# Optimization experiments

Hardware: AMD Instinct MI355X
Metric: run time of the kernel (lower is better)

The kernel has to match this reference:

```python
import jax, jax.numpy as jnp
import numpy as np

EMBED_DIM = 768
NUM_HEADS = 12
HEAD_DIM = EMBED_DIM // NUM_HEADS
B, S = 2, 2048


def setup_inputs() -> dict:
    key = jax.random.key(0)
    k1, k2, k3, k4, k5 = jax.random.split(key, 5)
    scale = 1.0 / np.sqrt(EMBED_DIM)
    return {
        "x": jax.random.normal(k1, (B, S, EMBED_DIM), dtype=jnp.float32),
        "w_qkv": jax.random.normal(k2, (EMBED_DIM, 3 * EMBED_DIM), dtype=jnp.float32) * scale,
        "b_qkv": jax.random.normal(k3, (3 * EMBED_DIM,), dtype=jnp.float32) * 0.01,
        "w_proj": jax.random.normal(k4, (EMBED_DIM, EMBED_DIM), dtype=jnp.float32) * scale,
        "b_proj": jax.random.normal(k5, (EMBED_DIM,), dtype=jnp.float32) * 0.01,
    }


def reference(x, w_qkv, b_qkv, w_proj, b_proj):
    b, s, e = x.shape
    h, d = NUM_HEADS, HEAD_DIM
    # fused QKV projection: [b, s, 3, h, d]
    qkv = (x @ w_qkv + b_qkv).reshape(b, s, 3, h, d)
    q = qkv[:, :, 0].transpose(0, 2, 1, 3)  # [b, h, s, d]
    k = qkv[:, :, 1].transpose(0, 2, 1, 3)
    v = qkv[:, :, 2].transpose(0, 2, 1, 3)
    scores = jnp.einsum("bhqd,bhkd->bhqk", q, k) * (d ** -0.5)
    attn = jax.nn.softmax(scores, axis=-1)  # dropout is identity in eval mode
    out = jnp.einsum("bhqk,bhkd->bhqd", attn, v)
    out = out.transpose(0, 2, 1, 3).reshape(b, s, e)
    return out @ w_proj + b_proj
```

## Files before the change

### kernel.cpp

```cpp
#include <hip/hip_runtime.h>
#include <hip/hip_bf16.h>


typedef __bf16 bf16x8 __attribute__((ext_vector_type(8)));
typedef float f32x4 __attribute__((ext_vector_type(4)));
typedef unsigned short ushortx8 __attribute__((ext_vector_type(8)));
typedef unsigned short ushortx4 __attribute__((ext_vector_type(4)));

#define EMB 768
#define SEQ 2048
#define NHEAD 12
#define HDIM 64
#define MROWS 4096
#define NQKV 2304
#define QSCALE 0.18033688011112042f

static __device__ __forceinline__ unsigned short b16(float f) {
  __hip_bfloat16 h = __float2bfloat16(f);
  return __builtin_bit_cast(unsigned short, h);
}

static __device__ __forceinline__ void gld16(const void* g, void* l) {
  __builtin_amdgcn_global_load_lds((const __attribute__((address_space(1))) void*)g,
                                   (__attribute__((address_space(3))) void*)l, 16, 0, 0);
}

__global__ __launch_bounds__(256) void k_prep(
    const float* __restrict__ x, const float* __restrict__ wqkv, const float* __restrict__ wproj,
    unsigned short* __restrict__ xb, unsigned short* __restrict__ wqkvT,
    unsigned short* __restrict__ wprojT) {
  __shared__ float t[64][65];
  const int bid = blockIdx.x;
  if (bid < 3072) {
    int i = (bid * 256 + threadIdx.x) * 4;
    f32x4 v = *(const f32x4*)(x + i);
    ushortx4 o;
    o[0] = b16(v[0]); o[1] = b16(v[1]); o[2] = b16(v[2]); o[3] = b16(v[3]);
    *(ushortx4*)(xb + i) = o;
    return;
  }
  const float* in; unsigned short* out; int N, bx, by;
  if (bid < 3072 + 432) { in = wqkv;  out = wqkvT;  N = NQKV; int r = bid - 3072; bx = r % 36; by = r / 36; }
  else                  { in = wproj; out = wprojT; N = EMB;  int r = bid - 3504; bx = r % 12; by = r / 12; }
  const int n0 = bx * 64, k0 = by * 64;
  const int xx = threadIdx.x & 63, y0 = threadIdx.x >> 6;
  #pragma unroll
  for (int i = 0; i < 16; ++i) { int r = y0 * 16 + i; t[r][xx] = in[(size_t)(k0 + r) * N + n0 + xx]; }
  __syncthreads();
  #pragma unroll
  for (int i = 0; i < 16; ++i) { int r = y0 * 16 + i; out[(size_t)(n0 + r) * EMB + k0 + xx] = b16(t[xx][r]); }
}

static __device__ __forceinline__ void gemm_tile_128(
    const unsigned short* __restrict__ A, const unsigned short* __restrict__ B,
    int K, int bm, int bn, char* lA, char* lB, f32x4 acc[4][4]) {
  const int tid = threadIdx.x, lane = tid & 63, w = tid >> 6;
  const int l15 = lane & 15, lg = lane >> 4;
  const int wm = w >> 1, wn = w & 1;
  #pragma unroll
  for (int m = 0; m < 4; ++m)
    #pragma unroll
    for (int n = 0; n < 4; ++n)
      acc[m][n] = (f32x4){0.f, 0.f, 0.f, 0.f};

  const size_t aoff1 = (size_t)(bm * 128 + (tid >> 2)) * K + (tid & 3) * 8;
  const size_t aoff2 = aoff1 + (size_t)64 * K;
  const size_t boff1 = (size_t)(bn * 128 + (tid >> 2)) * K + (tid & 3) * 8;
  const size_t boff2 = boff1 + (size_t)64 * K;
  const char* aBase = lA + (wm * 64 + l15) * 64 + lg * 16;
  const char* bBase = lB + (wn * 64 + l15) * 64 + lg * 16;
  const int T = K >> 5;

  #define GSTAGE(tt, buf) do {                                   \
    char* ad_ = lA + (buf) * 8192 + w * 1024;                    \
    char* bd_ = lB + (buf) * 8192 + w * 1024;                    \
    const int k0_ = (tt) << 5;                                   \
    gld16(A + aoff1 + k0_, ad_);                                 \
    gld16(A + aoff2 + k0_, ad_ + 4096);                          \
    gld16(B + boff1 + k0_, bd_);                                 \
    gld16(B + boff2 + k0_, bd_ + 4096);                          \
  } while (0)

  GSTAGE(0, 0);
  GSTAGE(1, 1);
  asm volatile("s_waitcnt vmcnt(4)" ::: "memory");
  __builtin_amdgcn_s_barrier();

  int cur = 0, pre = 2;
  for (int t = 0; t < T; ++t) {
    if (t + 2 < T) GSTAGE(t + 2, pre);
    const char* ab = aBase + cur * 8192;
    const char* bb = bBase + cur * 8192;
    bf16x8 af[4], bfr[4];
    #pragma unroll
    for (int m = 0; m < 4; ++m) af[m] = *(const bf16x8*)(ab + m * 1024);
    #pragma unroll
    for (int n = 0; n < 4; ++n) bfr[n] = *(const bf16x8*)(bb + n * 1024);
    __builtin_amdgcn_s_setprio(1);
    #pragma unroll
    for (int m = 0; m < 4; ++m)
      #pragma unroll
      for (int n = 0; n < 4; ++n)
        acc[m][n] = __builtin_amdgcn_mfma_f32_16x16x32_bf16(af[m], bfr[n], acc[m][n], 0, 0, 0);
    __builtin_amdgcn_s_setprio(0);
    if (t + 1 < T) {
      if (t + 2 < T) asm volatile("s_waitcnt vmcnt(4)" ::: "memory");
      else           asm volatile("s_waitcnt vmcnt(0)" ::: "memory");
      __builtin_amdgcn_s_barrier();
    }
    cur = (cur == 2) ? 0 : cur + 1;
    pre = (pre == 2) ? 0 : pre + 1;
  }
  #undef GSTAGE
}

static __device__ __forceinline__ int kvperm(int s) {
  return (s & ~0x1C) | ((s & 0x0C) << 1) | ((s & 0x10) >> 2);
}

__global__ __launch_bounds__(256) void k_gemm_qkv(
    const unsigned short* __restrict__ Xb, const unsigned short* __restrict__ Wt,
    const float* __restrict__ bias,
    unsigned short* __restrict__ Qb, unsigned short* __restrict__ Kb,
    unsigned short* __restrict__ VTb) {
  __shared__ __align__(16) char Alds[3 * 8192];
  __shared__ __align__(16) char Blds[3 * 8192];
  f32x4 acc[4][4];
  const int bm = blockIdx.x, bn = blockIdx.y;
  gemm_tile_128(Xb, Wt, EMB, bm, bn, Alds, Blds, acc);
  const int tid = threadIdx.x, lane = tid & 63, w = tid >> 6;
  const int l15 = lane & 15, lg = lane >> 4, wm = w >> 1, wn = w & 1;
  const int treg = bn / 6;
  if (treg < 2) {
    #pragma unroll
    for (int m = 0; m < 4; ++m)
      #pragma unroll
      for (int n = 0; n < 4; ++n)
        #pragma unroll
        for (int r = 0; r < 4; ++r) {
          int gr = bm * 128 + wm * 64 + m * 16 + lg * 4 + r;
          int gc = bn * 128 + wn * 64 + n * 16 + l15;
          float v = acc[m][n][r] + bias[gc];
          int rem = gc - treg * 768;
          int h = rem >> 6, d = rem & 63;
          int b = gr >> 11, s = gr & 2047;
          size_t off = ((size_t)(b * 12 + h) * 2048 + s) * 64 + d;
          if (treg == 0) Qb[off] = b16(v * QSCALE);
          else           Kb[off] = b16(v);
        }
  } else {
    #pragma unroll
    for (int m = 0; m < 4; ++m)
      #pragma unroll
      for (int n = 0; n < 4; ++n) {
        int gr0 = bm * 128 + wm * 64 + m * 16 + lg * 4;
        int gc = bn * 128 + wn * 64 + n * 16 + l15;
        int rem = gc - 1536;
        int h = rem >> 6, d = rem & 63;
        int b = gr0 >> 11, s0 = gr0 & 2047;
        int sp0 = kvperm(s0);
        ushortx4 o;
        #pragma unroll
        for (int r = 0; r < 4; ++r) o[r] = b16(acc[m][n][r] + bias[gc]);
        *(ushortx4*)(VTb + ((size_t)(b * 12 + h) * 64 + d) * 2048 + sp0) = o;
      }
  }
}

__global__ __launch_bounds__(256) void k_gemm_proj(
    const unsigned short* __restrict__ Ab, const unsigned short* __restrict__ Wt,
    const float* __restrict__ bias, float* __restrict__ out) {
  __shared__ __align__(16) char Alds[3 * 8192];
  __shared__ __align__(16) char Blds[3 * 8192];
  f32x4 acc[4][4];
  const int bm = blockIdx.x, bn = blockIdx.y;
  gemm_tile_128(Ab, Wt, EMB, bm, bn, Alds, Blds, acc);
  const int tid = threadIdx.x, lane = tid & 63, w = tid >> 6;
  const int l15 = lane & 15, lg = lane >> 4, wm = w >> 1, wn = w & 1;
  #pragma unroll
  for (int m = 0; m < 4; ++m)
    #pragma unroll
    for (int n = 0; n < 4; ++n)
      #pragma unroll
      for (int r = 0; r < 4; ++r) {
        int gr = bm * 128 + wm * 64 + m * 16 + lg * 4 + r;
        int gc = bn * 128 + wn * 64 + n * 16 + l15;
        out[(size_t)gr * EMB + gc] = acc[m][n][r] + bias[gc];
      }
}

__global__ __launch_bounds__(256) void k_attn(
    const unsigned short* __restrict__ Qg, const unsigned short* __restrict__ Kg,
    const unsigned short* __restrict__ VTg, unsigned short* __restrict__ AO) {
  __shared__ __align__(16) char KL[3 * 8192];
  __shared__ __align__(16) char VTL[3 * 8192];
  const int bid = blockIdx.x;
  const int bh = bid >> 5, qt = bid & 31;
  const int b = bh / 12, h = bh % 12;
  const size_t base = (size_t)bh * (SEQ * HDIM);
  const int tid = threadIdx.x, lane = tid & 63, w = tid >> 6;
  const int l15 = lane & 15, lg = lane >> 4;
  const int swz = (l15 & 7) << 4;

  bf16x8 qf[2];
  {
    const size_t qoff = base + (size_t)(qt * 64 + w * 16 + l15) * 64 + lg * 8;
    qf[0] = *(const bf16x8*)(Qg + qoff);
    qf[1] = *(const bf16x8*)(Qg + qoff + 32);
  }

  const int srow0 = tid >> 3;
  const int scg0 = (tid & 7) ^ (srow0 & 7);
  const int scg1 = (tid & 7) ^ ((srow0 + 32) & 7);

  #define ASTAGE(tt, buf) do {                                                         \
    const int kv_ = (tt) * 64;                                                         \
    char* kd_ = KL + (buf) * 8192 + w * 1024;                                          \
    char* vd_ = VTL + (buf) * 8192 + w * 1024;                                         \
    gld16(Kg + base + (size_t)(kv_ + srow0) * 64 + scg0 * 8,           kd_);           \
    gld16(Kg + base + (size_t)(kv_ + srow0 + 32) * 64 + scg1 * 8,      kd_ + 4096);    \
    gld16(VTg + base + (size_t)srow0 * 2048 + kv_ + scg0 * 8,          vd_);           \
    gld16(VTg + base + (size_t)(srow0 + 32) * 2048 + kv_ + scg1 * 8,   vd_ + 4096);    \
  } while (0)

  f32x4 Oacc[4];
  #pragma unroll
  for (int nd = 0; nd < 4; ++nd) Oacc[nd] = (f32x4){0.f, 0.f, 0.f, 0.f};
  float l_ = 0.f;

  ASTAGE(0, 0);
  ASTAGE(1, 1);
  asm volatile("s_waitcnt vmcnt(4)" ::: "memory");
  __builtin_amdgcn_s_barrier();

  int cur = 0, pre = 2;
  for (int t = 0; t < 32; ++t) {
    if (t + 2 < 32) ASTAGE(t + 2, pre);
    const char* kb = KL + cur * 8192;
    const char* vb = VTL + cur * 8192;

    f32x4 sv[4];
    __builtin_amdgcn_s_setprio(1);
    #pragma unroll
    for (int n = 0; n < 4; ++n) {
      const char* rb = kb + (n * 16 + l15) * 128;
      bf16x8 kf0 = *(const bf16x8*)(rb + ((lg * 16) ^ swz));
      bf16x8 kf1 = *(const bf16x8*)(rb + ((64 + lg * 16) ^ swz));
      f32x4 z = (f32x4){0.f, 0.f, 0.f, 0.f};
      z = __builtin_amdgcn_mfma_f32_16x16x32_bf16(kf0, qf[0], z, 0, 0, 0);
      sv[n] = __builtin_amdgcn_mfma_f32_16x16x32_bf16(kf1, qf[1], z, 0, 0, 0);
    }

    #pragma unroll
    for (int c = 0; c < 2; ++c) {
      ushortx8 up;
      #pragma unroll
      for (int j = 0; j < 4; ++j) {
        float pa = __builtin_amdgcn_exp2f(sv[2 * c][j]);
        float pb = __builtin_amdgcn_exp2f(sv[2 * c + 1][j]);
        l_ += pa + pb;
        up[j] = b16(pa);
        up[4 + j] = b16(pb);
      }
      bf16x8 pfB = __builtin_bit_cast(bf16x8, up);
      #pragma unroll
      for (int nd = 0; nd < 4; ++nd) {
        const char* vr = vb + (nd * 16 + l15) * 128;
        bf16x8 vf = *(const bf16x8*)(vr + ((c * 64 + lg * 16) ^ swz));
        Oacc[nd] = __builtin_amdgcn_mfma_f32_16x16x32_bf16(vf, pfB, Oacc[nd], 0, 0, 0);
      }
    }
    __builtin_amdgcn_s_setprio(0);

    if (t < 31) {
      if (t < 30) asm volatile("s_waitcnt vmcnt(4)" ::: "memory");
      else        asm volatile("s_waitcnt vmcnt(0)" ::: "memory");
      __builtin_amdgcn_s_barrier();
    }
    cur = (cur == 2) ? 0 : cur + 1;
    pre = (pre == 2) ? 0 : pre + 1;
  }
  #undef ASTAGE

  l_ += __shfl_xor(l_, 16);
  l_ += __shfl_xor(l_, 32);
  const float rl = 1.0f / l_;
  const int q = qt * 64 + w * 16 + l15;
  #pragma unroll
  for (int nd = 0; nd < 4; ++nd) {
    ushortx4 o;
    #pragma unroll
    for (int r = 0; r < 4; ++r) o[r] = b16(Oacc[nd][r] * rl);
    *(ushortx4*)(AO + ((size_t)(b * 2048 + q)) * EMB + h * 64 + nd * 16 + lg * 4) = o;
  }
}

extern "C" void kernel_launch(void* const* d_in, const int* in_sizes, int n_in,
                              void* d_out, int out_size, void* d_ws, size_t ws_size,
                              hipStream_t stream) {
  const float* x     = (const float*)d_in[0];
  const float* wqkv  = (const float*)d_in[1];
  const float* bqkv  = (const float*)d_in[2];
  const float* wproj = (const float*)d_in[3];
  const float* bproj = (const float*)d_in[4];
  float* out = (float*)d_out;
  char* ws = (char*)d_ws;

  unsigned short* xb     = (unsigned short*)(ws + 0);
  unsigned short* wqkvT  = (unsigned short*)(ws + 6291456);
  unsigned short* wprojT = (unsigned short*)(ws + 9830400);
  unsigned short* Qb     = (unsigned short*)(ws + 11010048);
  unsigned short* Kb     = (unsigned short*)(ws + 17301504);
  unsigned short* VTb    = (unsigned short*)(ws + 23592960);
  unsigned short* AOb    = (unsigned short*)(ws + 29884416);

  k_prep<<<3648, 256, 0, stream>>>(x, wqkv, wproj, xb, wqkvT, wprojT);
  k_gemm_qkv<<<dim3(MROWS / 128, NQKV / 128), 256, 0, stream>>>(xb, wqkvT, bqkv, Qb, Kb, VTb);
  k_attn<<<24 * (SEQ / 64), 256, 0, stream>>>(Qb, Kb, VTb, AOb);
  k_gemm_proj<<<dim3(MROWS / 128, EMB / 128), 256, 0, stream>>>(AOb, wprojT, bproj, out);
}
```

Baseline: 106.6 us.

## Software-pipeline attention PV with next QK, remap blocks per XCD, unroll GEMM

The attention loop is restructured so the PV MFMAs for the previous tile overlap with the QK and exp work for the current tile. The row sum is now computed by an MFMA against a ones vector instead of VALU adds and shuffles. All three kernels remap block IDs so related tiles land on the same XCD (id&7), aiming at better L2 reuse. The GEMM K loop is fully unrolled with a compile-time K and setprio is dropped there. The costs are higher register pressure from holding the V fragments, and the row sum now accumulates bf16-rounded probabilities.

```diff
diff --git a/kernel.cpp b/kernel.cpp
--- a/kernel.cpp
+++ b/kernel.cpp
@@ -53,7 +53,7 @@
 
 static __device__ __forceinline__ void gemm_tile_128(
     const unsigned short* __restrict__ A, const unsigned short* __restrict__ B,
-    int K, int bm, int bn, char* lA, char* lB, f32x4 acc[4][4]) {
+    int bm, int bn, char* lA, char* lB, f32x4 acc[4][4]) {
   const int tid = threadIdx.x, lane = tid & 63, w = tid >> 6;
   const int l15 = lane & 15, lg = lane >> 4;
   const int wm = w >> 1, wn = w & 1;
@@ -63,13 +63,12 @@
     for (int n = 0; n < 4; ++n)
       acc[m][n] = (f32x4){0.f, 0.f, 0.f, 0.f};
 
-  const size_t aoff1 = (size_t)(bm * 128 + (tid >> 2)) * K + (tid & 3) * 8;
-  const size_t aoff2 = aoff1 + (size_t)64 * K;
-  const size_t boff1 = (size_t)(bn * 128 + (tid >> 2)) * K + (tid & 3) * 8;
-  const size_t boff2 = boff1 + (size_t)64 * K;
+  const size_t aoff1 = (size_t)(bm * 128 + (tid >> 2)) * EMB + (tid & 3) * 8;
+  const size_t aoff2 = aoff1 + (size_t)64 * EMB;
+  const size_t boff1 = (size_t)(bn * 128 + (tid >> 2)) * EMB + (tid & 3) * 8;
+  const size_t boff2 = boff1 + (size_t)64 * EMB;
   const char* aBase = lA + (wm * 64 + l15) * 64 + lg * 16;
   const char* bBase = lB + (wn * 64 + l15) * 64 + lg * 16;
-  const int T = K >> 5;
 
   #define GSTAGE(tt, buf) do {                                   \
     char* ad_ = lA + (buf) * 8192 + w * 1024;                    \
@@ -86,9 +85,10 @@
   asm volatile("s_waitcnt vmcnt(4)" ::: "memory");
   __builtin_amdgcn_s_barrier();
 
-  int cur = 0, pre = 2;
-  for (int t = 0; t < T; ++t) {
-    if (t + 2 < T) GSTAGE(t + 2, pre);
+  #pragma unroll
+  for (int t = 0; t < 24; ++t) {
+    const int cur = t % 3;
+    if (t + 2 < 24) GSTAGE(t + 2, (t + 2) % 3);
     const char* ab = aBase + cur * 8192;
     const char* bb = bBase + cur * 8192;
     bf16x8 af[4], bfr[4];
@@ -96,20 +96,16 @@
     for (int m = 0; m < 4; ++m) af[m] = *(const bf16x8*)(ab + m * 1024);
     #pragma unroll
     for (int n = 0; n < 4; ++n) bfr[n] = *(const bf16x8*)(bb + n * 1024);
-    __builtin_amdgcn_s_setprio(1);
     #pragma unroll
     for (int m = 0; m < 4; ++m)
       #pragma unroll
       for (int n = 0; n < 4; ++n)
         acc[m][n] = __builtin_amdgcn_mfma_f32_16x16x32_bf16(af[m], bfr[n], acc[m][n], 0, 0, 0);
-    __builtin_amdgcn_s_setprio(0);
-    if (t + 1 < T) {
-      if (t + 2 < T) asm volatile("s_waitcnt vmcnt(4)" ::: "memory");
-      else           asm volatile("s_waitcnt vmcnt(0)" ::: "memory");
+    if (t + 1 < 24) {
+      if (t + 2 < 24) asm volatile("s_waitcnt vmcnt(4)" ::: "memory");
+      else            asm volatile("s_waitcnt vmcnt(0)" ::: "memory");
       __builtin_amdgcn_s_barrier();
     }
-    cur = (cur == 2) ? 0 : cur + 1;
-    pre = (pre == 2) ? 0 : pre + 1;
   }
   #undef GSTAGE
 }
@@ -126,8 +122,11 @@
   __shared__ __align__(16) char Alds[3 * 8192];
   __shared__ __align__(16) char Blds[3 * 8192];
   f32x4 acc[4][4];
-  const int bm = blockIdx.x, bn = blockIdx.y;
-  gemm_tile_128(Xb, Wt, EMB, bm, bn, Alds, Blds, acc);
+  const int id = blockIdx.x;
+  const int k = id >> 3;
+  const int bn = k % 18;
+  const int bm = (id & 7) * 4 + k / 18;
+  gemm_tile_128(Xb, Wt, bm, bn, Alds, Blds, acc);
   const int tid = threadIdx.x, lane = tid & 63, w = tid >> 6;
   const int l15 = lane & 15, lg = lane >> 4, wm = w >> 1, wn = w & 1;
   const int treg = bn / 6;
@@ -173,8 +172,11 @@
   __shared__ __align__(16) char Alds[3 * 8192];
   __shared__ __align__(16) char Blds[3 * 8192];
   f32x4 acc[4][4];
-  const int bm = blockIdx.x, bn = blockIdx.y;
-  gemm_tile_128(Ab, Wt, EMB, bm, bn, Alds, Blds, acc);
+  const int id = blockIdx.x;
+  const int k = id >> 3;
+  const int bn = k % 6;
+  const int bm = (id & 7) * 4 + k / 6;
+  gemm_tile_128(Ab, Wt, bm, bn, Alds, Blds, acc);
   const int tid = threadIdx.x, lane = tid & 63, w = tid >> 6;
   const int l15 = lane & 15, lg = lane >> 4, wm = w >> 1, wn = w & 1;
   #pragma unroll
@@ -195,7 +197,9 @@
   __shared__ __align__(16) char KL[3 * 8192];
   __shared__ __align__(16) char VTL[3 * 8192];
   const int bid = blockIdx.x;
-  const int bh = bid >> 5, qt = bid & 31;
+  const int slot = bid >> 3;
+  const int bh = (bid & 7) * 3 + slot / 32;
+  const int qt = slot & 31;
   const int b = bh / 12, h = bh % 12;
   const size_t base = (size_t)bh * (SEQ * HDIM);
   const int tid = threadIdx.x, lane = tid & 63, w = tid >> 6;
@@ -223,68 +227,98 @@
     gld16(VTg + base + (size_t)(srow0 + 32) * 2048 + kv_ + scg1 * 8,   vd_ + 4096);    \
   } while (0)
 
+  ushortx8 os;
+  #pragma unroll
+  for (int j = 0; j < 8; ++j) os[j] = 0x3F80;
+  const bf16x8 onesf = __builtin_bit_cast(bf16x8, os);
+
   f32x4 Oacc[4];
   #pragma unroll
   for (int nd = 0; nd < 4; ++nd) Oacc[nd] = (f32x4){0.f, 0.f, 0.f, 0.f};
-  float l_ = 0.f;
+  f32x4 Lacc = (f32x4){0.f, 0.f, 0.f, 0.f};
+  bf16x8 pf0, pf1;
+  bf16x8 vf[8];
+
+  #define QK_EXP(kb_) do {                                                             \
+    f32x4 sv[4];                                                                       \
+    _Pragma("unroll")                                                                  \
+    for (int n = 0; n < 4; ++n) {                                                      \
+      const char* rb = (kb_) + (n * 16 + l15) * 128;                                   \
+      bf16x8 kf0 = *(const bf16x8*)(rb + ((lg * 16) ^ swz));                           \
+      bf16x8 kf1 = *(const bf16x8*)(rb + ((64 + lg * 16) ^ swz));                      \
+      f32x4 z = (f32x4){0.f, 0.f, 0.f, 0.f};                                           \
+      z = __builtin_amdgcn_mfma_f32_16x16x32_bf16(kf0, qf[0], z, 0, 0, 0);             \
+      sv[n] = __builtin_amdgcn_mfma_f32_16x16x32_bf16(kf1, qf[1], z, 0, 0, 0);         \
+    }                                                                                  \
+    ushortx8 u0, u1;                                                                   \
+    _Pragma("unroll")                                                                  \
+    for (int j = 0; j < 4; ++j) {                                                      \
+      u0[j]     = b16(__builtin_amdgcn_exp2f(sv[0][j]));                               \
+      u0[4 + j] = b16(__builtin_amdgcn_exp2f(sv[1][j]));                               \
+      u1[j]     = b16(__builtin_amdgcn_exp2f(sv[2][j]));                               \
+      u1[4 + j] = b16(__builtin_amdgcn_exp2f(sv[3][j]));                               \
+    }                                                                                  \
+    pf0 = __builtin_bit_cast(bf16x8, u0);                                              \
+    pf1 = __builtin_bit_cast(bf16x8, u1);                                              \
+  } while (0)
+
+  #define VREAD(vb_) do {                                                              \
+    _Pragma("unroll")                                                                  \
+    for (int c = 0; c < 2; ++c)                                                        \
+      _Pragma("unroll")                                                                \
+      for (int nd = 0; nd < 4; ++nd)                                                   \
+        vf[c * 4 + nd] = *(const bf16x8*)((vb_) + (nd * 16 + l15) * 128 +              \
+                                          ((c * 64 + lg * 16) ^ swz));                 \
+  } while (0)
+
+  #define PV_PREV() do {                                                               \
+    Lacc = __builtin_amdgcn_mfma_f32_16x16x32_bf16(onesf, pf0, Lacc, 0, 0, 0);         \
+    Lacc = __builtin_amdgcn_mfma_f32_16x16x32_bf16(onesf, pf1, Lacc, 0, 0, 0);         \
+    _Pragma("unroll")                                                                  \
+    for (int nd = 0; nd < 4; ++nd)                                                     \
+      Oacc[nd] = __builtin_amdgcn_mfma_f32_16x16x32_bf16(vf[nd], pf0, Oacc[nd], 0,0,0);\
+    _Pragma("unroll")                                                                  \
+    for (int nd = 0; nd < 4; ++nd)                                                     \
+      Oacc[nd] = __builtin_amdgcn_mfma_f32_16x16x32_bf16(vf[4+nd], pf1, Oacc[nd],0,0,0);\
+  } while (0)
 
   ASTAGE(0, 0);
   ASTAGE(1, 1);
   asm volatile("s_waitcnt vmcnt(4)" ::: "memory");
   __builtin_amdgcn_s_barrier();
 
-  int cur = 0, pre = 2;
-  for (int t = 0; t < 32; ++t) {
-    if (t + 2 < 32) ASTAGE(t + 2, pre);
+  ASTAGE(2, 2);
+  QK_EXP(KL);
+  VREAD(VTL);
+  asm volatile("s_waitcnt lgkmcnt(0)" ::: "memory");
+  asm volatile("s_waitcnt vmcnt(4)" ::: "memory");
+  __builtin_amdgcn_s_barrier();
+
+  for (int t = 1; t < 32; ++t) {
+    const int cur = t % 3;
+    if (t + 2 < 32) ASTAGE(t + 2, (t + 2) % 3);
     const char* kb = KL + cur * 8192;
     const char* vb = VTL + cur * 8192;
-
-    f32x4 sv[4];
     __builtin_amdgcn_s_setprio(1);
-    #pragma unroll
-    for (int n = 0; n < 4; ++n) {
-      const char* rb = kb + (n * 16 + l15) * 128;
-      bf16x8 kf0 = *(const bf16x8*)(rb + ((lg * 16) ^ swz));
-      bf16x8 kf1 = *(const bf16x8*)(rb + ((64 + lg * 16) ^ swz));
-      f32x4 z = (f32x4){0.f, 0.f, 0.f, 0.f};
-      z = __builtin_amdgcn_mfma_f32_16x16x32_bf16(kf0, qf[0], z, 0, 0, 0);
-      sv[n] = __builtin_amdgcn_mfma_f32_16x16x32_bf16(kf1, qf[1], z, 0, 0, 0);
-    }
-
-    #pragma unroll
-    for (int c = 0; c < 2; ++c) {
-      ushortx8 up;
-      #pragma unroll
-      for (int j = 0; j < 4; ++j) {
-        float pa = __builtin_amdgcn_exp2f(sv[2 * c][j]);
-        float pb = __builtin_amdgcn_exp2f(sv[2 * c + 1][j]);
-        l_ += pa + pb;
-        up[j] = b16(pa);
-        up[4 + j] = b16(pb);
-      }
-      bf16x8 pfB = __builtin_bit_cast(bf16x8, up);
-      #pragma unroll
-      for (int nd = 0; nd < 4; ++nd) {
-        const char* vr = vb + (nd * 16 + l15) * 128;
-        bf16x8 vf = *(const bf16x8*)(vr + ((c * 64 + lg * 16) ^ swz));
-        Oacc[nd] = __builtin_amdgcn_mfma_f32_16x16x32_bf16(vf, pfB, Oacc[nd], 0, 0, 0);
-      }
-    }
+    PV_PREV();
+    QK_EXP(kb);
     __builtin_amdgcn_s_setprio(0);
-
+    VREAD(vb);
     if (t < 31) {
+      asm volatile("s_waitcnt lgkmcnt(0)" ::: "memory");
       if (t < 30) asm volatile("s_waitcnt vmcnt(4)" ::: "memory");
       else        asm volatile("s_waitcnt vmcnt(0)" ::: "memory");
       __builtin_amdgcn_s_barrier();
     }
-    cur = (cur == 2) ? 0 : cur + 1;
-    pre = (pre == 2) ? 0 : pre + 1;
-  }
+  }
+  PV_PREV();
+
   #undef ASTAGE
-
-  l_ += __shfl_xor(l_, 16);
-  l_ += __shfl_xor(l_, 32);
-  const float rl = 1.0f / l_;
+  #undef QK_EXP
+  #undef VREAD
+  #undef PV_PREV
+
+  const float rl = 1.0f / Lacc[0];
   const int q = qt * 64 + w * 16 + l15;
   #pragma unroll
   for (int nd = 0; nd < 4; ++nd) {
@@ -315,7 +349,7 @@
   unsigned short* AOb    = (unsigned short*)(ws + 29884416);
 
   k_prep<<<3648, 256, 0, stream>>>(x, wqkv, wproj, xb, wqkvT, wprojT);
-  k_gemm_qkv<<<dim3(MROWS / 128, NQKV / 128), 256, 0, stream>>>(xb, wqkvT, bqkv, Qb, Kb, VTb);
+  k_gemm_qkv<<<576, 256, 0, stream>>>(xb, wqkvT, bqkv, Qb, Kb, VTb);
   k_attn<<<24 * (SEQ / 64), 256, 0, stream>>>(Qb, Kb, VTb, AOb);
-  k_gemm_proj<<<dim3(MROWS / 128, EMB / 128), 256, 0, stream>>>(AOb, wprojT, bproj, out);
-}
+  k_gemm_proj<<<192, 256, 0, stream>>>(AOb, wprojT, bproj, out);
+}
```

Result: faster. 96.99 us (-9.0%).
